# Optimization experiments

Hardware: AMD Instinct MI355X
Metric: run time of the kernel (lower is better)

The kernel has to match this reference:

```python
import jax, jax.numpy as jnp
import numpy as np

NUM_WIRES = 14
N_LAYERS = 2
BATCH = 256
DIM = 2 ** NUM_WIRES


def setup_inputs() -> dict:
    key = jax.random.key(0)
    k1, k2, k3 = jax.random.split(key, 3)
    s = jax.random.normal(k1, (BATCH, DIM), dtype=jnp.float32)
    # StatePrep requires normalized amplitudes
    s = s / jnp.linalg.norm(s, axis=1, keepdims=True)
    params = jax.random.normal(k2, (N_LAYERS, NUM_WIRES, 3), dtype=jnp.float32)
    head_w = jax.random.normal(k3, (1, NUM_WIRES), dtype=jnp.float32) / np.sqrt(NUM_WIRES)
    head_b = jnp.zeros((1,), dtype=jnp.float32)
    return {"state_batch": s, "params": params, "head_w": head_w, "head_b": head_b}


def _ry(t):
    c = jnp.cos(t / 2).astype(jnp.complex64)
    s = jnp.sin(t / 2).astype(jnp.complex64)
    return jnp.stack([jnp.stack([c, -s]), jnp.stack([s, c])])


def _rz(t):
    tc = t.astype(jnp.complex64)
    e_m = jnp.exp(-0.5j * tc)
    e_p = jnp.exp(0.5j * tc)
    z = jnp.zeros((), jnp.complex64)
    return jnp.stack([jnp.stack([e_m, z]), jnp.stack([z, e_p])])


def _rx(t):
    c = jnp.cos(t / 2).astype(jnp.complex64)
    s = (-1j) * jnp.sin(t / 2).astype(jnp.complex64)
    return jnp.stack([jnp.stack([c, s]), jnp.stack([s, c])])


def _apply_1q(psi, U, wire):
    # psi: (B, 2, 2, ..., 2); contract 2x2 gate on axis wire+1 across the batch
    out = jnp.tensordot(U, psi, axes=([1], [wire + 1]))
    return jnp.moveaxis(out, 0, wire + 1)


def _apply_cnot(psi, control, target):
    # flip target axis where control bit == 1
    shape = [1] * psi.ndim
    shape[control + 1] = 2
    mask = (jnp.arange(2) == 1).reshape(shape)
    return jnp.where(mask, jnp.flip(psi, axis=target + 1), psi)


def _circuit(state_c, params):
    psi = state_c.reshape((BATCH,) + (2,) * NUM_WIRES)
    for layer in range(N_LAYERS):
        for w in range(NUM_WIRES):
            psi = _apply_1q(psi, _ry(params[layer, w, 0]), w)
            psi = _apply_1q(psi, _rz(params[layer, w, 1]), w)
            psi = _apply_cnot(psi, w, (w + 1) % NUM_WIRES)
            psi = _apply_1q(psi, _rx(params[layer, w, 2]), w)
    probs = (psi.real ** 2 + psi.imag ** 2).reshape(BATCH, DIM)
    # <Z_w> = sum over basis states of prob * (+1/-1 depending on bit of wire w)
    basis = jnp.arange(DIM)
    shifts = NUM_WIRES - 1 - jnp.arange(NUM_WIRES)  # wire 0 is the MSB axis
    signs = 1.0 - 2.0 * ((basis[None, :] >> shifts[:, None]) & 1).astype(jnp.float32)
    return probs @ signs.T  # (B, NUM_WIRES)


def reference(state_batch, params, head_w, head_b):
    feats = _circuit(state_batch.astype(jnp.complex64), params)  # (B, NUM_WIRES)
    return feats @ head_w[0] + head_b[0]  # (B,)
```

## Files before the change

### kernel.cpp

```cpp
#include <hip/hip_runtime.h>
#include <math.h>

typedef float v2f __attribute__((ext_vector_type(2)));

constexpr int NW = 14;
constexpr int DIM = 1 << NW;
constexpr int BATCH = 256;
constexpr int NT = 1024;

__device__ __host__ constexpr int swz(int i) {
    return i ^ (((i >> 5) & 15) << 1) ^ (((i >> 9) & 15) << 1) ^ (((i >> 13) & 1) << 1);
}

template<int Q0,int Q1,int Q2,int Q3,int Q4,int Q5,int Q6,int Q7,int Q8,int Q9>
__device__ __forceinline__ int scat10(int t) {
    return ((t & 1) << Q0) | (((t >> 1) & 1) << Q1) | (((t >> 2) & 1) << Q2) |
           (((t >> 3) & 1) << Q3) | (((t >> 4) & 1) << Q4) | (((t >> 5) & 1) << Q5) |
           (((t >> 6) & 1) << Q6) | (((t >> 7) & 1) << Q7) | (((t >> 8) & 1) << Q8) |
           (((t >> 9) & 1) << Q9);
}

__device__ __forceinline__ v2f pkmul_lo(v2f P, v2f B) {
    v2f d; asm("v_pk_mul_f32 %0, %1, %2 op_sel:[0,0] op_sel_hi:[0,1]"
               : "=v"(d) : "v"(P), "v"(B)); return d;
}
__device__ __forceinline__ v2f pkmul_hi(v2f P, v2f B) {
    v2f d; asm("v_pk_mul_f32 %0, %1, %2 op_sel:[1,0] op_sel_hi:[1,1]"
               : "=v"(d) : "v"(P), "v"(B)); return d;
}
__device__ __forceinline__ v2f pkfma_lo(v2f P, v2f B, v2f C) {
    v2f d; asm("v_pk_fma_f32 %0, %1, %2, %3 op_sel:[0,0,0] op_sel_hi:[0,1,1]"
               : "=v"(d) : "v"(P), "v"(B), "v"(C)); return d;
}
__device__ __forceinline__ v2f pkfma_hi(v2f P, v2f B, v2f C) {
    v2f d; asm("v_pk_fma_f32 %0, %1, %2, %3 op_sel:[1,0,0] op_sel_hi:[1,1,1]"
               : "=v"(d) : "v"(P), "v"(B), "v"(C)); return d;
}
__device__ __forceinline__ v2f pkfmn_hi(v2f P, v2f B, v2f C) {
    v2f d; asm("v_pk_fma_f32 %0, %1, %2, %3 op_sel:[1,0,0] op_sel_hi:[1,1,1] neg_lo:[1,0,0] neg_hi:[1,0,0]"
               : "=v"(d) : "v"(P), "v"(B), "v"(C)); return d;
}

template<int JW, int JT>
__device__ __forceinline__ void gate_u(v2f (&pr)[8], v2f (&pi)[8],
                                       v2f Y, v2f Z, v2f X)
{
    constexpr int BW = 1 << JW, BT = 1 << JT, JF = 3 - JW - JT;
    #pragma unroll
    for (int m = 0; m < 2; ++m) {
        const int l00 = m << JF;
        const int iA = l00, iB = l00 | BW, iC = l00 | BT, iD = l00 | BW | BT;

        v2f a00r = pr[iA], a00i = pi[iA];
        v2f a10r = pr[iB], a10i = pi[iB];
        v2f a01r = pr[iC], a01i = pi[iC];
        v2f a11r = pr[iD], a11i = pi[iD];

        v2f v0r = pkfmn_hi(Y, a10r, pkmul_lo(Y, a00r));
        v2f v0i = pkfmn_hi(Y, a10i, pkmul_lo(Y, a00i));
        v2f v1r = pkfma_lo(Y, a10r, pkmul_hi(Y, a00r));
        v2f v1i = pkfma_lo(Y, a10i, pkmul_hi(Y, a00i));
        v2f u0r = pkfmn_hi(Y, a11r, pkmul_lo(Y, a01r));
        v2f u0i = pkfmn_hi(Y, a11i, pkmul_lo(Y, a01i));
        v2f u1r = pkfma_lo(Y, a11r, pkmul_hi(Y, a01r));
        v2f u1i = pkfma_lo(Y, a11i, pkmul_hi(Y, a01i));

        v2f b00r = pkfma_hi(Z, v0i, pkmul_lo(Z, v0r));
        v2f b00i = pkfmn_hi(Z, v0r, pkmul_lo(Z, v0i));
        v2f b10r = pkfmn_hi(Z, v1i, pkmul_lo(Z, v1r));
        v2f b10i = pkfma_hi(Z, v1r, pkmul_lo(Z, v1i));
        v2f b01r = pkfma_hi(Z, u0i, pkmul_lo(Z, u0r));
        v2f b01i = pkfmn_hi(Z, u0r, pkmul_lo(Z, u0i));
        v2f b11r = pkfmn_hi(Z, u1i, pkmul_lo(Z, u1r));
        v2f b11i = pkfma_hi(Z, u1r, pkmul_lo(Z, u1i));

        pr[iA] = pkfma_hi(X, b11i, pkmul_lo(X, b00r));
        pi[iA] = pkfmn_hi(X, b11r, pkmul_lo(X, b00i));
        pr[iB] = pkfma_lo(X, b11r, pkmul_hi(X, b00i));
        pi[iB] = pkfmn_hi(X, b00r, pkmul_lo(X, b11i));
        pr[iC] = pkfma_hi(X, b10i, pkmul_lo(X, b01r));
        pi[iC] = pkfmn_hi(X, b10r, pkmul_lo(X, b01i));
        pr[iD] = pkfma_lo(X, b10r, pkmul_hi(X, b01i));
        pi[iD] = pkfmn_hi(X, b01r, pkmul_lo(X, b10i));
    }
}

template<int J>
__device__ __forceinline__ void swap_l5(v2f (&pr)[8], v2f (&pi)[8]) {
    constexpr int jA = (J == 0) ? 1 : 0, jB = (J == 2) ? 1 : 2;
    #pragma unroll
    for (int m = 0; m < 4; ++m) {
        const int l0 = ((m & 1) << jA) | (((m >> 1) & 1) << jB);
        const int l1 = l0 | (1 << J);
        { float a=pr[l0].x, c=pr[l1].x; asm("s_nop 1\n\tv_permlane32_swap_b32 %0, %1":"+v"(a),"+v"(c)); pr[l0].x=a; pr[l1].x=c; }
        { float a=pr[l0].y, c=pr[l1].y; asm("s_nop 1\n\tv_permlane32_swap_b32 %0, %1":"+v"(a),"+v"(c)); pr[l0].y=a; pr[l1].y=c; }
        { float a=pi[l0].x, c=pi[l1].x; asm("s_nop 1\n\tv_permlane32_swap_b32 %0, %1":"+v"(a),"+v"(c)); pi[l0].x=a; pi[l1].x=c; }
        { float a=pi[l0].y, c=pi[l1].y; asm("s_nop 1\n\tv_permlane32_swap_b32 %0, %1":"+v"(a),"+v"(c)); pi[l0].y=a; pi[l1].y=c; }
    }
}

template<int J>
__device__ __forceinline__ void swap_l4(v2f (&pr)[8], v2f (&pi)[8]) {
    constexpr int jA = (J == 0) ? 1 : 0, jB = (J == 2) ? 1 : 2;
    #pragma unroll
    for (int m = 0; m < 4; ++m) {
        const int l0 = ((m & 1) << jA) | (((m >> 1) & 1) << jB);
        const int l1 = l0 | (1 << J);
        { float a=pr[l0].x, c=pr[l1].x; asm("s_nop 1\n\tv_permlane16_swap_b32 %0, %1":"+v"(a),"+v"(c)); pr[l0].x=a; pr[l1].x=c; }
        { float a=pr[l0].y, c=pr[l1].y; asm("s_nop 1\n\tv_permlane16_swap_b32 %0, %1":"+v"(a),"+v"(c)); pr[l0].y=a; pr[l1].y=c; }
        { float a=pi[l0].x, c=pi[l1].x; asm("s_nop 1\n\tv_permlane16_swap_b32 %0, %1":"+v"(a),"+v"(c)); pi[l0].x=a; pi[l1].x=c; }
        { float a=pi[l0].y, c=pi[l1].y; asm("s_nop 1\n\tv_permlane16_swap_b32 %0, %1":"+v"(a),"+v"(c)); pi[l0].y=a; pi[l1].y=c; }
    }
}

template<int S0,int S1,int S2>
__device__ __forceinline__ void store64(float* re, float* im,
                                        const v2f (&pr)[8], const v2f (&pi)[8], int sb) {
    #pragma unroll
    for (int k = 0; k < 8; ++k) {
        const int c = swz(((k & 1) << S0) | (((k >> 1) & 1) << S1) | (((k >> 2) & 1) << S2));
        const int a = sb ^ c;
        *(v2f*)(re + a) = pr[k];
        *(v2f*)(im + a) = pi[k];
    }
}

template<int S0,int S1,int S2>
__device__ __forceinline__ void load64(const float* re, const float* im,
                                       v2f (&pr)[8], v2f (&pi)[8], int sb) {
    #pragma unroll
    for (int k = 0; k < 8; ++k) {
        const int c = swz(((k & 1) << S0) | (((k >> 1) & 1) << S1) | (((k >> 2) & 1) << S2));
        const int a = sb ^ c;
        pr[k] = *(const v2f*)(re + a);
        pi[k] = *(const v2f*)(im + a);
    }
}

template<int S0,int S1,int S2>
__device__ __forceinline__ void store32(float* re, float* im,
                                        const v2f (&pr)[8], const v2f (&pi)[8], int sb) {
    #pragma unroll
    for (int k = 0; k < 8; ++k) {
        const int cc = ((k & 1) << S0) | (((k >> 1) & 1) << S1) | (((k >> 2) & 1) << S2);
        const int a0 = sb ^ swz(cc);
        const int a1 = sb ^ swz(cc | 32);
        re[a0] = pr[k].x; re[a1] = pr[k].y;
        im[a0] = pi[k].x; im[a1] = pi[k].y;
    }
}

template<int S0,int S1,int S2>
__device__ __forceinline__ void load32(const float* re, const float* im,
                                       v2f (&pr)[8], v2f (&pi)[8], int sb) {
    #pragma unroll
    for (int k = 0; k < 8; ++k) {
        const int cc = ((k & 1) << S0) | (((k >> 1) & 1) << S1) | (((k >> 2) & 1) << S2);
        const int a0 = sb ^ swz(cc);
        const int a1 = sb ^ swz(cc | 32);
        pr[k].x = re[a0]; pr[k].y = re[a1];
        pi[k].x = im[a0]; pi[k].y = im[a1];
    }
}

__global__ __launch_bounds__(NT, 1) void qsim(const float* __restrict__ state,
                                              const float* __restrict__ params,
                                              const float* __restrict__ head_w,
                                              const float* __restrict__ head_b,
                                              float* __restrict__ out)
{
    __shared__ float re[DIM];
    __shared__ float im[DIM];
    __shared__ float2 csv[NW * 3 * 2];
    __shared__ float partial[NT / 64];

    const int t = threadIdx.x;
    const int b = blockIdx.x;

    v2f pr[8], pi[8];

    const float2* __restrict__ sp2 = (const float2*)(state + (size_t)b * DIM);
    const int tb1 = scat10<1,2,3,4,9,10,5,6,7,8>(t);
    #pragma unroll
    for (int k = 0; k < 8; ++k) {
        const int idx = tb1 | ((k & 1) << 11) | (((k >> 1) & 1) << 12) | (((k >> 2) & 1) << 13);
        const float2 v = sp2[idx >> 1];
        pr[k] = v2f{v.x, v.y};
        pi[k] = v2f{0.0f, 0.0f};
    }

    if (t < NW * 3 * 2) {
        float sv, cv;
        sincosf(params[t] * 0.5f, &sv, &cv);
        csv[t] = make_float2(cv, sv);
    }
    __syncthreads();

#define GU(JW, JT, G) do {                                              \
        v2f Y = *(const v2f*)&csv[(G)*3+0];                             \
        v2f Z = *(const v2f*)&csv[(G)*3+1];                             \
        v2f X = *(const v2f*)&csv[(G)*3+2];                             \
        gate_u<JW, JT>(pr, pi, Y, Z, X);                                \
    } while (0)

    GU(2, 1, 0);
    GU(1, 0, 1);
    swap_l5<2>(pr, pi);
    GU(0, 2, 2);
    swap_l4<1>(pr, pi);
    GU(2, 1, 3);
    store64<11,9,10>(re, im, pr, pi, swz(scat10<1,2,3,4,12,13,5,6,7,8>(t)));
    __syncthreads();

    load64<7,8,9>(re, im, pr, pi, swz(scat10<1,2,3,4,5,6,13,12,11,10>(t)));
    GU(2, 1, 4);
    GU(1, 0, 5);
    swap_l5<2>(pr, pi);
    GU(0, 2, 6);
    swap_l4<1>(pr, pi);
    GU(2, 1, 7);
    store64<7,5,6>(re, im, pr, pi, swz(scat10<1,2,3,4,8,9,13,12,11,10>(t)));
    __syncthreads();

    load64<3,4,5>(re, im, pr, pi, swz(scat10<13,6,7,8,1,2,12,11,10,9>(t)));
    GU(2, 1, 8);
    GU(1, 0, 9);
    swap_l5<2>(pr, pi);
    GU(0, 2, 10);
    swap_l4<1>(pr, pi);
    GU(2, 1, 11);
    store64<3,1,2>(re, im, pr, pi, swz(scat10<13,6,7,8,4,5,12,11,10,9>(t)));
    __syncthreads();

    load32<13,0,1>(re, im, pr, pi, swz(scat10<2,3,4,9,11,12,10,8,7,6>(t)));
    GU(2, 1, 12);
    GU(1, 0, 13);
    swap_l5<2>(pr, pi);
    GU(0, 2, 14);
    swap_l4<1>(pr, pi);
    GU(2, 1, 15);
    store32<13,11,12>(re, im, pr, pi, swz(scat10<2,3,4,9,0,1,10,8,7,6>(t)));
    __syncthreads();

    load64<9,10,11>(re, im, pr, pi, swz(scat10<1,2,3,4,7,8,13,12,6,5>(t)));
    GU(2, 1, 16);
    GU(1, 0, 17);
    swap_l5<2>(pr, pi);
    GU(0, 2, 18);
    swap_l4<1>(pr, pi);
    GU(2, 1, 19);
    store64<9,7,8>(re, im, pr, pi, swz(scat10<1,2,3,4,10,11,13,12,6,5>(t)));
    __syncthreads();

    load64<5,6,7>(re, im, pr, pi, swz(scat10<1,2,11,8,3,4,13,12,10,9>(t)));
    GU(2, 1, 20);
    GU(1, 0, 21);
    swap_l5<2>(pr, pi);
    GU(0, 2, 22);
    swap_l4<1>(pr, pi);
    GU(2, 1, 23);
    store64<5,3,4>(re, im, pr, pi, swz(scat10<1,2,11,8,6,7,13,12,10,9>(t)));
    __syncthreads();

    load32<1,2,3>(re, im, pr, pi, swz(scat10<9,10,11,12,13,0,8,7,6,4>(t)));
    GU(2, 1, 24);
    GU(1, 0, 25);
    swap_l5<2>(pr, pi);
    GU(0, 2, 26);
    swap_l4<1>(pr, pi);
    GU(2, 1, 27);

    float hw[NW];
    #pragma unroll
    for (int w = 0; w < NW; ++w) hw[w] = head_w[w];

    float gbase = 0.0f;
    gbase += (t & 1)   ? -hw[4]  : hw[4];
    gbase += (t & 2)   ? -hw[3]  : hw[3];
    gbase += (t & 4)   ? -hw[2]  : hw[2];
    gbase += (t & 8)   ? -hw[1]  : hw[1];
    gbase += (t & 16)  ? -hw[11] : hw[11];
    gbase += (t & 32)  ? -hw[10] : hw[10];
    gbase += (t & 64)  ? -hw[5]  : hw[5];
    gbase += (t & 128) ? -hw[6]  : hw[6];
    gbase += (t & 256) ? -hw[7]  : hw[7];
    gbase += (t & 512) ? -hw[9]  : hw[9];

    v2f acc2 = {0.0f, 0.0f};
    #pragma unroll
    for (int k = 0; k < 8; ++k) {
        float g = gbase;
        g += (k & 1) ? -hw[12] : hw[12];
        g += (k & 2) ? -hw[0]  : hw[0];
        g += (k & 4) ? -hw[13] : hw[13];
        v2f gv = {g + hw[8], g - hw[8]};
        acc2 += (pr[k]*pr[k] + pi[k]*pi[k]) * gv;
    }
    float acc = acc2.x + acc2.y;

    #pragma unroll
    for (int off = 32; off > 0; off >>= 1) acc += __shfl_down(acc, off);
    if ((t & 63) == 0) partial[t >> 6] = acc;
    __syncthreads();
    if (t == 0) {
        float tot = 0.0f;
        #pragma unroll
        for (int k = 0; k < NT / 64; ++k) tot += partial[k];
        out[b] = tot + head_b[0];
    }
#undef GU
}

extern "C" void kernel_launch(void* const* d_in, const int* in_sizes, int n_in,
                              void* d_out, int out_size, void* d_ws, size_t ws_size,
                              hipStream_t stream) {
    const float* state  = (const float*)d_in[0];
    const float* params = (const float*)d_in[1];
    const float* head_w = (const float*)d_in[2];
    const float* head_b = (const float*)d_in[3];
    float* outp = (float*)d_out;
    qsim<<<BATCH, NT, 0, stream>>>(state, params, head_w, head_b, outp);
}
```

Measured before the change: 37.64 us.

## Reorder qubit mapping so consecutive stages reuse thread-private LDS slots without barriers

```diff
diff --git a/kernel.cpp b/kernel.cpp
--- a/kernel.cpp
+++ b/kernel.cpp
@@ -137,27 +137,27 @@
     }
 }
 
-template<int S0,int S1,int S2>
+template<int S0,int S1,int S2,int PB>
 __device__ __forceinline__ void store32(float* re, float* im,
                                         const v2f (&pr)[8], const v2f (&pi)[8], int sb) {
     #pragma unroll
     for (int k = 0; k < 8; ++k) {
         const int cc = ((k & 1) << S0) | (((k >> 1) & 1) << S1) | (((k >> 2) & 1) << S2);
         const int a0 = sb ^ swz(cc);
-        const int a1 = sb ^ swz(cc | 32);
+        const int a1 = sb ^ swz(cc | (1 << PB));
         re[a0] = pr[k].x; re[a1] = pr[k].y;
         im[a0] = pi[k].x; im[a1] = pi[k].y;
     }
 }
 
-template<int S0,int S1,int S2>
+template<int S0,int S1,int S2,int PB>
 __device__ __forceinline__ void load32(const float* re, const float* im,
                                        v2f (&pr)[8], v2f (&pi)[8], int sb) {
     #pragma unroll
     for (int k = 0; k < 8; ++k) {
         const int cc = ((k & 1) << S0) | (((k >> 1) & 1) << S1) | (((k >> 2) & 1) << S2);
         const int a0 = sb ^ swz(cc);
-        const int a1 = sb ^ swz(cc | 32);
+        const int a1 = sb ^ swz(cc | (1 << PB));
         pr[k].x = re[a0]; pr[k].y = re[a1];
         pi[k].x = im[a0]; pi[k].y = im[a1];
     }
@@ -180,10 +180,10 @@
     v2f pr[8], pi[8];
 
     const float2* __restrict__ sp2 = (const float2*)(state + (size_t)b * DIM);
-    const int tb1 = scat10<1,2,3,4,9,10,5,6,7,8>(t);
-    #pragma unroll
-    for (int k = 0; k < 8; ++k) {
-        const int idx = tb1 | ((k & 1) << 11) | (((k >> 1) & 1) << 12) | (((k >> 2) & 1) << 13);
+    const int tbA = scat10<1,2,3,4,9,10,5,6,7,8>(t);
+    #pragma unroll
+    for (int k = 0; k < 8; ++k) {
+        const int idx = tbA | ((k & 1) << 13) | (((k >> 1) & 1) << 12) | (((k >> 2) & 1) << 11);
         const float2 v = sp2[idx >> 1];
         pr[k] = v2f{v.x, v.y};
         pi[k] = v2f{0.0f, 0.0f};
@@ -203,97 +203,99 @@
         gate_u<JW, JT>(pr, pi, Y, Z, X);                                \
     } while (0)
 
-    GU(2, 1, 0);
-    GU(1, 0, 1);
-    swap_l5<2>(pr, pi);
-    GU(0, 2, 2);
+    GU(0, 1, 0);
+    GU(1, 2, 1);
+    swap_l5<0>(pr, pi);
+    GU(2, 0, 2);
     swap_l4<1>(pr, pi);
-    GU(2, 1, 3);
-    store64<11,9,10>(re, im, pr, pi, swz(scat10<1,2,3,4,12,13,5,6,7,8>(t)));
-    __syncthreads();
-
-    load64<7,8,9>(re, im, pr, pi, swz(scat10<1,2,3,4,5,6,13,12,11,10>(t)));
-    GU(2, 1, 4);
-    GU(1, 0, 5);
-    swap_l5<2>(pr, pi);
-    GU(0, 2, 6);
-    swap_l4<1>(pr, pi);
-    GU(2, 1, 7);
-    store64<7,5,6>(re, im, pr, pi, swz(scat10<1,2,3,4,8,9,13,12,11,10>(t)));
-    __syncthreads();
-
-    load64<3,4,5>(re, im, pr, pi, swz(scat10<13,6,7,8,1,2,12,11,10,9>(t)));
-    GU(2, 1, 8);
-    GU(1, 0, 9);
-    swap_l5<2>(pr, pi);
-    GU(0, 2, 10);
-    swap_l4<1>(pr, pi);
-    GU(2, 1, 11);
-    store64<3,1,2>(re, im, pr, pi, swz(scat10<13,6,7,8,4,5,12,11,10,9>(t)));
-    __syncthreads();
-
-    load32<13,0,1>(re, im, pr, pi, swz(scat10<2,3,4,9,11,12,10,8,7,6>(t)));
-    GU(2, 1, 12);
-    GU(1, 0, 13);
-    swap_l5<2>(pr, pi);
-    GU(0, 2, 14);
-    swap_l4<1>(pr, pi);
-    GU(2, 1, 15);
-    store32<13,11,12>(re, im, pr, pi, swz(scat10<2,3,4,9,0,1,10,8,7,6>(t)));
-    __syncthreads();
-
-    load64<9,10,11>(re, im, pr, pi, swz(scat10<1,2,3,4,7,8,13,12,6,5>(t)));
-    GU(2, 1, 16);
-    GU(1, 0, 17);
-    swap_l5<2>(pr, pi);
-    GU(0, 2, 18);
-    swap_l4<1>(pr, pi);
-    GU(2, 1, 19);
-    store64<9,7,8>(re, im, pr, pi, swz(scat10<1,2,3,4,10,11,13,12,6,5>(t)));
-    __syncthreads();
-
-    load64<5,6,7>(re, im, pr, pi, swz(scat10<1,2,11,8,3,4,13,12,10,9>(t)));
-    GU(2, 1, 20);
-    GU(1, 0, 21);
-    swap_l5<2>(pr, pi);
-    GU(0, 2, 22);
-    swap_l4<1>(pr, pi);
-    GU(2, 1, 23);
-    store64<5,3,4>(re, im, pr, pi, swz(scat10<1,2,11,8,6,7,13,12,10,9>(t)));
-    __syncthreads();
-
-    load32<1,2,3>(re, im, pr, pi, swz(scat10<9,10,11,12,13,0,8,7,6,4>(t)));
-    GU(2, 1, 24);
-    GU(1, 0, 25);
-    swap_l5<2>(pr, pi);
-    GU(0, 2, 26);
-    swap_l4<1>(pr, pi);
-    GU(2, 1, 27);
+    GU(0, 1, 3);
+    store64<10,9,11>(re, im, pr, pi, swz(scat10<1,2,3,4,12,13,5,6,7,8>(t)));
+    __syncthreads();
+
+    load64<9,8,7>(re, im, pr, pi, swz(scat10<4,3,2,1,6,5,13,12,11,10>(t)));
+    GU(0, 1, 4);
+    GU(1, 2, 5);
+    swap_l4<0>(pr, pi);
+    GU(2, 0, 6);
+    swap_l5<1>(pr, pi);
+    GU(0, 1, 7);
+    store64<6,5,7>(re, im, pr, pi, swz(scat10<4,3,2,1,9,8,13,12,11,10>(t)));
+    asm volatile("" ::: "memory");
+    load64<5,4,3>(re, im, pr, pi, swz(scat10<7,6,9,8,2,1,13,12,11,10>(t)));
+    GU(0, 1, 8);
+    GU(1, 2, 9);
+    swap_l4<0>(pr, pi);
+    GU(2, 0, 10);
+    swap_l5<1>(pr, pi);
+    GU(0, 1, 11);
+    store64<2,1,3>(re, im, pr, pi, swz(scat10<7,6,9,8,5,4,13,12,11,10>(t)));
+    __syncthreads();
+
+    load32<1,0,13,4>(re, im, pr, pi, swz(scat10<3,2,10,9,12,11,8,7,6,5>(t)));
+    GU(0, 1, 12);
+    GU(1, 2, 13);
+    swap_l4<0>(pr, pi);
+    GU(2, 0, 14);
+    swap_l5<1>(pr, pi);
+    GU(0, 1, 15);
+    store32<12,11,13,4>(re, im, pr, pi, swz(scat10<3,2,10,9,1,0,8,7,6,5>(t)));
+    asm volatile("" ::: "memory");
+    {
+        const int sbC2 = swz(scat10<3,2,13,12,1,0,8,7,6,5>(t));
+        load32<11,10,9,4>(re, im, pr, pi, sbC2);
+        GU(0, 1, 16);
+        GU(1, 2, 17);
+        store32<11,10,9,4>(re, im, pr, pi, sbC2);
+    }
+    __syncthreads();
+
+    load64<9,8,7>(re, im, pr, pi, swz(scat10<4,3,2,1,6,5,13,12,11,10>(t)));
+    GU(0, 1, 18);
+    GU(1, 2, 19);
+    swap_l4<0>(pr, pi);
+    GU(2, 0, 20);
+    swap_l5<1>(pr, pi);
+    GU(0, 1, 21);
+    store64<6,5,7>(re, im, pr, pi, swz(scat10<4,3,2,1,9,8,13,12,11,10>(t)));
+    asm volatile("" ::: "memory");
+    load64<5,4,3>(re, im, pr, pi, swz(scat10<7,6,9,8,2,1,13,12,11,10>(t)));
+    GU(0, 1, 22);
+    GU(1, 2, 23);
+    swap_l4<0>(pr, pi);
+    GU(2, 0, 24);
+    swap_l5<1>(pr, pi);
+    GU(0, 1, 25);
+    store64<2,1,3>(re, im, pr, pi, swz(scat10<7,6,9,8,5,4,13,12,11,10>(t)));
+    __syncthreads();
+
+    load32<1,0,13,2>(re, im, pr, pi, swz(scat10<8,7,6,5,4,3,12,11,10,9>(t)));
+    GU(0, 1, 26);
+    GU(1, 2, 27);
 
     float hw[NW];
     #pragma unroll
     for (int w = 0; w < NW; ++w) hw[w] = head_w[w];
 
     float gbase = 0.0f;
-    gbase += (t & 1)   ? -hw[4]  : hw[4];
-    gbase += (t & 2)   ? -hw[3]  : hw[3];
-    gbase += (t & 4)   ? -hw[2]  : hw[2];
-    gbase += (t & 8)   ? -hw[1]  : hw[1];
-    gbase += (t & 16)  ? -hw[11] : hw[11];
+    gbase += (t & 1)   ? -hw[5]  : hw[5];
+    gbase += (t & 2)   ? -hw[6]  : hw[6];
+    gbase += (t & 4)   ? -hw[7]  : hw[7];
+    gbase += (t & 8)   ? -hw[8]  : hw[8];
+    gbase += (t & 16)  ? -hw[9]  : hw[9];
     gbase += (t & 32)  ? -hw[10] : hw[10];
-    gbase += (t & 64)  ? -hw[5]  : hw[5];
-    gbase += (t & 128) ? -hw[6]  : hw[6];
-    gbase += (t & 256) ? -hw[7]  : hw[7];
-    gbase += (t & 512) ? -hw[9]  : hw[9];
+    gbase += (t & 64)  ? -hw[1]  : hw[1];
+    gbase += (t & 128) ? -hw[2]  : hw[2];
+    gbase += (t & 256) ? -hw[3]  : hw[3];
+    gbase += (t & 512) ? -hw[4]  : hw[4];
 
     v2f acc2 = {0.0f, 0.0f};
     #pragma unroll
     for (int k = 0; k < 8; ++k) {
         float g = gbase;
         g += (k & 1) ? -hw[12] : hw[12];
-        g += (k & 2) ? -hw[0]  : hw[0];
-        g += (k & 4) ? -hw[13] : hw[13];
-        v2f gv = {g + hw[8], g - hw[8]};
+        g += (k & 2) ? -hw[13] : hw[13];
+        g += (k & 4) ? -hw[0]  : hw[0];
+        v2f gv = {g + hw[11], g - hw[11]};
         acc2 += (pr[k]*pr[k] + pi[k]*pi[k]) * gv;
     }
     float acc = acc2.x + acc2.y;
```

Result: slower. 39.02 us (+3.7%).
